# Performance work log

Measured on AMD Instinct MI355X. Metric: run time of the kernel, lower is better.

Reference implementation:

```python
import jax, jax.numpy as jnp
import numpy as np

B, S, D, H = 4, 2048, 768, 12
HD = D // H  # head_dim = 64


def setup_inputs() -> dict:
    key = jax.random.key(0)
    k1, k2, k3, k4, k5 = jax.random.split(key, 5)
    scale = 0.02
    return {
        "x": jax.random.normal(k1, (B, S, D), dtype=jnp.float32),
        "w_qkv": jax.random.normal(k2, (D, 3 * D), dtype=jnp.float32) * scale,
        "b_qkv": jax.random.normal(k3, (3 * D,), dtype=jnp.float32) * scale,
        "w_proj": jax.random.normal(k4, (D, D), dtype=jnp.float32) * scale,
        "b_proj": jax.random.normal(k5, (D,), dtype=jnp.float32) * scale,
    }


def reference(x, w_qkv, b_qkv, w_proj, b_proj):
    b, s, d = x.shape
    # fused qkv projection: (b, s, 3d) -> (3, b, h, s, hd)
    qkv = x @ w_qkv + b_qkv
    qkv = qkv.reshape(b, s, 3, H, HD).transpose(2, 0, 3, 1, 4)
    q, k, v = qkv[0], qkv[1], qkv[2]
    # scaled dot-product attention with explicit (b, h, s, s) scores
    scores = jnp.einsum("bhqd,bhkd->bhqk", q, k) / jnp.sqrt(jnp.float32(HD))
    attn = jax.nn.softmax(scores, axis=-1)
    out = jnp.einsum("bhqk,bhkd->bhqd", attn, v)
    out = out.transpose(0, 2, 1, 3).reshape(b, s, d)  # concat heads
    return out @ w_proj + b_proj
```

## Files before the change

kernel.cpp:

```cpp
#include <hip/hip_runtime.h>
#include <hip/hip_bf16.h>
#include <stdint.h>


typedef __attribute__((ext_vector_type(8))) short bf16x8;
typedef __attribute__((ext_vector_type(4))) float f32x4;
typedef __attribute__((ext_vector_type(4))) unsigned short u16x4;

__device__ __forceinline__ unsigned short f2bf(float x) {
  union { float f; uint32_t u; } v; v.f = x;
  uint32_t r = v.u + 0x7FFF + ((v.u >> 16) & 1);
  return (unsigned short)(r >> 16);
}

__device__ __forceinline__ uint32_t cvtpk_bf16(float lo, float hi) {
  uint32_t r;
  asm("v_cvt_pk_bf16_f32 %0, %1, %2" : "=v"(r) : "v"(lo), "v"(hi));
  return r;
}

__device__ __forceinline__ void gload_lds16(const void* g, void* l) {
  __builtin_amdgcn_global_load_lds(
      (const __attribute__((address_space(1))) void*)g,
      (__attribute__((address_space(3))) void*)l, 16, 0, 0);
}

__global__ void cast_x_kernel(const float* __restrict__ x,
                              unsigned short* __restrict__ xb, int n) {
  int idx = (blockIdx.x * blockDim.x + threadIdx.x) * 4;
  if (idx < n) {
    f32x4 v = *(const f32x4*)(x + idx);
    u16x4 o;
    o[0] = f2bf(v[0]); o[1] = f2bf(v[1]); o[2] = f2bf(v[2]); o[3] = f2bf(v[3]);
    *(u16x4*)(xb + idx) = o;
  }
}

__global__ void transpose_cast_kernel(const float* __restrict__ W,
                                      unsigned short* __restrict__ Wt,
                                      int K, int N) {
  __shared__ float tile[64][65];
  int k0 = blockIdx.y * 64, n0 = blockIdx.x * 64;
  int t = threadIdx.x;
#pragma unroll
  for (int i = 0; i < 16; i++) {
    int idx = i * 256 + t; int r = idx >> 6, c = idx & 63;
    tile[r][c] = W[(size_t)(k0 + r) * N + n0 + c];
  }
  __syncthreads();
#pragma unroll
  for (int i = 0; i < 16; i++) {
    int idx = i * 256 + t; int r = idx >> 6, c = idx & 63;
    Wt[(size_t)(n0 + r) * K + k0 + c] = f2bf(tile[c][r]);
  }
}

template <int EPI>
__global__ __launch_bounds__(256, 2) void gemm_kernel(
    const unsigned short* __restrict__ A,
    const unsigned short* __restrict__ Bt,
    const float* __restrict__ bias,
    void* __restrict__ out0,
    unsigned short* __restrict__ Kb,
    unsigned short* __restrict__ Vt,
    int M, int N, int K) {
  __shared__ unsigned short As[128 * 64];
  __shared__ unsigned short Bs[128 * 64];
  const int tid = threadIdx.x;
  const int wave = tid >> 6, lane = tid & 63;
  const int wm = wave >> 1, wn = wave & 1;
  const int m0 = blockIdx.y * 128, n0 = blockIdx.x * 128;
  const int g = lane >> 4, c16 = lane & 15;
  f32x4 acc[4][4] = {};

  for (int k0 = 0; k0 < K; k0 += 64) {
    int rb = wave * 32;
#pragma unroll
    for (int j = 0; j < 4; j++) {
      int r = rb + j * 8 + (lane >> 3);
      int ca = (lane & 7) ^ (r & 7);
      gload_lds16(A + (size_t)(m0 + r) * K + k0 + ca * 8, As + (rb + j * 8) * 64);
      gload_lds16(Bt + (size_t)(n0 + r) * K + k0 + ca * 8, Bs + (rb + j * 8) * 64);
    }
    __syncthreads();
#pragma unroll
    for (int ks = 0; ks < 2; ks++) {
      bf16x8 af[4], bfr[4];
#pragma unroll
      for (int mi = 0; mi < 4; mi++) {
        int row = wm * 64 + mi * 16 + c16;
        int ch = (ks * 4 + g) ^ (row & 7);
        af[mi] = *(const bf16x8*)(As + row * 64 + ch * 8);
      }
#pragma unroll
      for (int nj = 0; nj < 4; nj++) {
        int row = wn * 64 + nj * 16 + c16;
        int ch = (ks * 4 + g) ^ (row & 7);
        bfr[nj] = *(const bf16x8*)(Bs + row * 64 + ch * 8);
      }
#pragma unroll
      for (int mi = 0; mi < 4; mi++)
#pragma unroll
        for (int nj = 0; nj < 4; nj++)
          acc[mi][nj] = __builtin_amdgcn_mfma_f32_16x16x32_bf16(
              af[mi], bfr[nj], acc[mi][nj], 0, 0, 0);
    }
    __syncthreads();
  }

  if (EPI == 0) {
    const float QSC = 0.125f * 1.44269504088896f;
    unsigned short* Qb = (unsigned short*)out0;
#pragma unroll
    for (int nj = 0; nj < 4; nj++) {
      int n = n0 + wn * 64 + nj * 16 + c16;
      int t = n / 768, rr = n % 768;
      int h = rr >> 6, d = rr & 63;
      float bv = bias[n];
#pragma unroll
      for (int mi = 0; mi < 4; mi++) {
        int mrow = m0 + wm * 64 + mi * 16 + g * 4;
        int b = mrow >> 11, s = mrow & 2047;
        if (t == 0) {
          size_t base = ((size_t)(b * 12 + h) * 2048 + s) * 64 + d;
#pragma unroll
          for (int rg = 0; rg < 4; rg++)
            Qb[base + (size_t)rg * 64] = f2bf((acc[mi][nj][rg] + bv) * QSC);
        } else if (t == 1) {
          size_t base = ((size_t)(b * 12 + h) * 2048 + s) * 64 + d;
#pragma unroll
          for (int rg = 0; rg < 4; rg++)
            Kb[base + (size_t)rg * 64] = f2bf(acc[mi][nj][rg] + bv);
        } else {
          int sp = (s & ~31) + (((s >> 2) & 3) << 3) + (((s >> 4) & 1) << 2);
          u16x4 p;
          p[0] = f2bf(acc[mi][nj][0] + bv);
          p[1] = f2bf(acc[mi][nj][1] + bv);
          p[2] = f2bf(acc[mi][nj][2] + bv);
          p[3] = f2bf(acc[mi][nj][3] + bv);
          *(u16x4*)(Vt + ((size_t)(b * 12 + h) * 64 + d) * 2048 + sp) = p;
        }
      }
    }
  } else {
    float* outp = (float*)out0;
#pragma unroll
    for (int nj = 0; nj < 4; nj++) {
      int n = n0 + wn * 64 + nj * 16 + c16;
      float bv = bias[n];
#pragma unroll
      for (int mi = 0; mi < 4; mi++) {
        int mrow = m0 + wm * 64 + mi * 16 + g * 4;
#pragma unroll
        for (int rg = 0; rg < 4; rg++)
          outp[(size_t)(mrow + rg) * N + n] = acc[mi][nj][rg] + bv;
      }
    }
  }
}

__global__ __launch_bounds__(256, 4) void attn_kernel(
    const unsigned short* __restrict__ Qb,
    const unsigned short* __restrict__ Kb,
    const unsigned short* __restrict__ Vt,
    unsigned short* __restrict__ Ao) {
  __shared__ unsigned short Ks[64 * 64];
  __shared__ unsigned short Vs[64 * 64];
  const int id = blockIdx.x;
  const int xcd = id & 7, slot = id >> 3;
  const int bh = xcd * 6 + (slot % 6);
  const int q0 = (slot / 6) * 128;
  const int tid = threadIdx.x;
  const int wave = tid >> 6, lane = tid & 63;
  const int g = lane >> 4, c16 = lane & 15;
  const int rw = c16 & 7;
  const int rb = wave * 16;

  const int sr = rb + (lane >> 3);
  const int sca = (lane & 7) ^ (sr & 7);
  const unsigned short* kp = Kb + ((size_t)bh * 2048 + sr) * 64 + sca * 8;
  const unsigned short* vp = Vt + ((size_t)bh * 64 + sr) * 2048 + sca * 8;

  bf16x8 qf[2][2];
  {
    const unsigned short* qp =
        Qb + ((size_t)bh * 2048 + q0 + wave * 32 + c16) * 64;
#pragma unroll
    for (int qa = 0; qa < 2; qa++) {
      qf[qa][0] = *(const bf16x8*)(qp + qa * 1024 + g * 8);
      qf[qa][1] = *(const bf16x8*)(qp + qa * 1024 + 32 + g * 8);
    }
  }
  f32x4 acc_o[2][4] = {};
  float l_run[2] = {0.f, 0.f};
  const int alane = (lane & 48) + g * 4;

  for (int kt = 0; kt < 32; kt++) {
    gload_lds16(kp, Ks + rb * 64);
    gload_lds16(kp + 8 * 64, Ks + (rb + 8) * 64);
    gload_lds16(vp, Vs + rb * 64);
    gload_lds16(vp + 8 * 2048, Vs + (rb + 8) * 64);
    kp += 64 * 64;
    vp += 64;
    __syncthreads();

    f32x4 sacc[2][4] = {};
#pragma unroll
    for (int ks = 0; ks < 2; ks++) {
#pragma unroll
      for (int nf = 0; nf < 4; nf++) {
        int row = nf * 16 + c16;
        int ch = (ks * 4 + g) ^ (row & 7);
        bf16x8 kf = *(const bf16x8*)(Ks + row * 64 + ch * 8);
        sacc[0][nf] =
            __builtin_amdgcn_mfma_f32_16x16x32_bf16(kf, qf[0][ks], sacc[0][nf], 0, 0, 0);
        sacc[1][nf] =
            __builtin_amdgcn_mfma_f32_16x16x32_bf16(kf, qf[1][ks], sacc[1][nf], 0, 0, 0);
      }
    }

#pragma unroll
    for (int qa = 0; qa < 2; qa++) {
      float rs = 0.f;
#pragma unroll
      for (int nf = 0; nf < 4; nf++) {
        sacc[qa][nf][0] = __builtin_amdgcn_exp2f(sacc[qa][nf][0]);
        sacc[qa][nf][1] = __builtin_amdgcn_exp2f(sacc[qa][nf][1]);
        sacc[qa][nf][2] = __builtin_amdgcn_exp2f(sacc[qa][nf][2]);
        sacc[qa][nf][3] = __builtin_amdgcn_exp2f(sacc[qa][nf][3]);
        rs += (sacc[qa][nf][0] + sacc[qa][nf][1]) +
              (sacc[qa][nf][2] + sacc[qa][nf][3]);
      }
      l_run[qa] += rs;
    }

#pragma unroll
    for (int ks = 0; ks < 2; ks++) {
      union { uint32_t w[4]; bf16x8 v8; } pa0, pa1;
      pa0.w[0] = cvtpk_bf16(sacc[0][2 * ks][0], sacc[0][2 * ks][1]);
      pa0.w[1] = cvtpk_bf16(sacc[0][2 * ks][2], sacc[0][2 * ks][3]);
      pa0.w[2] = cvtpk_bf16(sacc[0][2 * ks + 1][0], sacc[0][2 * ks + 1][1]);
      pa0.w[3] = cvtpk_bf16(sacc[0][2 * ks + 1][2], sacc[0][2 * ks + 1][3]);
      pa1.w[0] = cvtpk_bf16(sacc[1][2 * ks][0], sacc[1][2 * ks][1]);
      pa1.w[1] = cvtpk_bf16(sacc[1][2 * ks][2], sacc[1][2 * ks][3]);
      pa1.w[2] = cvtpk_bf16(sacc[1][2 * ks + 1][0], sacc[1][2 * ks + 1][1]);
      pa1.w[3] = cvtpk_bf16(sacc[1][2 * ks + 1][2], sacc[1][2 * ks + 1][3]);
#pragma unroll
      for (int nf = 0; nf < 4; nf++) {
        int row = nf * 16 + c16;
        int ch = (ks * 4 + g) ^ rw;
        bf16x8 vf = *(const bf16x8*)(&Vs[row * 64 + ch * 8]);
        acc_o[0][nf] =
            __builtin_amdgcn_mfma_f32_16x16x32_bf16(pa0.v8, vf, acc_o[0][nf], 0, 0, 0);
        acc_o[1][nf] =
            __builtin_amdgcn_mfma_f32_16x16x32_bf16(pa1.v8, vf, acc_o[1][nf], 0, 0, 0);
      }
    }
    __syncthreads();
  }

  const int b = bh / 12, h = bh % 12;
#pragma unroll
  for (int qa = 0; qa < 2; qa++) {
    float t = l_run[qa];
    t += __shfl_xor(t, 16);
    t += __shfl_xor(t, 32);
    float l_q[4];
#pragma unroll
    for (int rg = 0; rg < 4; rg++)
      l_q[rg] = __shfl(t, alane + rg);
#pragma unroll
    for (int nf = 0; nf < 4; nf++) {
#pragma unroll
      for (int rg = 0; rg < 4; rg++) {
        float v = acc_o[qa][nf][rg] / l_q[rg];
        int srow = q0 + wave * 32 + qa * 16 + g * 4 + rg;
        Ao[((size_t)(b * 2048 + srow)) * 768 + h * 64 + nf * 16 + c16] = f2bf(v);
      }
    }
  }
}

extern "C" void kernel_launch(void* const* d_in, const int* in_sizes, int n_in,
                              void* d_out, int out_size, void* d_ws, size_t ws_size,
                              hipStream_t stream) {
  const float* x      = (const float*)d_in[0];
  const float* w_qkv  = (const float*)d_in[1];
  const float* b_qkv  = (const float*)d_in[2];
  const float* w_proj = (const float*)d_in[3];
  const float* b_proj = (const float*)d_in[4];

  unsigned short* xb  = (unsigned short*)d_ws;
  unsigned short* wqt = xb + 6291456;
  unsigned short* wpt = wqt + 1769472;
  unsigned short* Qb  = wpt + 589824;
  unsigned short* Kb  = Qb + 6291456;
  unsigned short* Vt  = Kb + 6291456;
  unsigned short* Ao  = Vt + 6291456;

  cast_x_kernel<<<6144, 256, 0, stream>>>(x, xb, 6291456);
  transpose_cast_kernel<<<dim3(36, 12), 256, 0, stream>>>(w_qkv, wqt, 768, 2304);
  transpose_cast_kernel<<<dim3(12, 12), 256, 0, stream>>>(w_proj, wpt, 768, 768);

  gemm_kernel<0><<<dim3(18, 64), 256, 0, stream>>>(
      xb, wqt, b_qkv, (void*)Qb, Kb, Vt, 8192, 2304, 768);

  attn_kernel<<<768, 256, 0, stream>>>(Qb, Kb, Vt, Ao);

  gemm_kernel<1><<<dim3(6, 64), 256, 0, stream>>>(
      Ao, wpt, b_proj, d_out, nullptr, nullptr, 8192, 768, 768);
}
```

Before: 143.7 us.

## Use two waves per attention block with 64 query rows per wave

The attention kernel drops from four waves to two per 128-query block, and each wave now handles 64 query rows instead of 32. Each K/V fragment read from LDS is reused across four query sub-tiles instead of two, so LDS read traffic per MFMA is halved. Each wave also issues twice as many global-to-LDS loads per tile. The cost is higher register pressure from the larger accumulators, plus fewer waves per block and a launch bound of 2, which may reduce occupancy and latency hiding.

```diff
diff --git a/kernel.cpp b/kernel.cpp
--- a/kernel.cpp
+++ b/kernel.cpp
@@ -159,7 +159,7 @@
   }
 }
 
-__global__ __launch_bounds__(256, 4) void attn_kernel(
+__global__ __launch_bounds__(128, 2) void attn_kernel(
     const unsigned short* __restrict__ Qb,
     const unsigned short* __restrict__ Kb,
     const unsigned short* __restrict__ Vt,
@@ -174,37 +174,40 @@
   const int wave = tid >> 6, lane = tid & 63;
   const int g = lane >> 4, c16 = lane & 15;
   const int rw = c16 & 7;
-  const int rb = wave * 16;
-
-  const int sr = rb + (lane >> 3);
+
+  const int sr = wave * 32 + (lane >> 3);
   const int sca = (lane & 7) ^ (sr & 7);
   const unsigned short* kp = Kb + ((size_t)bh * 2048 + sr) * 64 + sca * 8;
   const unsigned short* vp = Vt + ((size_t)bh * 64 + sr) * 2048 + sca * 8;
 
-  bf16x8 qf[2][2];
+  bf16x8 qf[4][2];
   {
     const unsigned short* qp =
-        Qb + ((size_t)bh * 2048 + q0 + wave * 32 + c16) * 64;
-#pragma unroll
-    for (int qa = 0; qa < 2; qa++) {
+        Qb + ((size_t)bh * 2048 + q0 + wave * 64 + c16) * 64;
+#pragma unroll
+    for (int qa = 0; qa < 4; qa++) {
       qf[qa][0] = *(const bf16x8*)(qp + qa * 1024 + g * 8);
       qf[qa][1] = *(const bf16x8*)(qp + qa * 1024 + 32 + g * 8);
     }
   }
-  f32x4 acc_o[2][4] = {};
-  float l_run[2] = {0.f, 0.f};
+  f32x4 acc_o[4][4] = {};
+  float l_run[4] = {0.f, 0.f, 0.f, 0.f};
   const int alane = (lane & 48) + g * 4;
 
   for (int kt = 0; kt < 32; kt++) {
-    gload_lds16(kp, Ks + rb * 64);
-    gload_lds16(kp + 8 * 64, Ks + (rb + 8) * 64);
-    gload_lds16(vp, Vs + rb * 64);
-    gload_lds16(vp + 8 * 2048, Vs + (rb + 8) * 64);
+    gload_lds16(kp, Ks + (wave * 32) * 64);
+    gload_lds16(kp + 8 * 64, Ks + (wave * 32 + 8) * 64);
+    gload_lds16(kp + 16 * 64, Ks + (wave * 32 + 16) * 64);
+    gload_lds16(kp + 24 * 64, Ks + (wave * 32 + 24) * 64);
+    gload_lds16(vp, Vs + (wave * 32) * 64);
+    gload_lds16(vp + 8 * 2048, Vs + (wave * 32 + 8) * 64);
+    gload_lds16(vp + 16 * 2048, Vs + (wave * 32 + 16) * 64);
+    gload_lds16(vp + 24 * 2048, Vs + (wave * 32 + 24) * 64);
     kp += 64 * 64;
     vp += 64;
     __syncthreads();
 
-    f32x4 sacc[2][4] = {};
+    f32x4 sacc[4][4] = {};
 #pragma unroll
     for (int ks = 0; ks < 2; ks++) {
 #pragma unroll
@@ -212,15 +215,15 @@
         int row = nf * 16 + c16;
         int ch = (ks * 4 + g) ^ (row & 7);
         bf16x8 kf = *(const bf16x8*)(Ks + row * 64 + ch * 8);
-        sacc[0][nf] =
-            __builtin_amdgcn_mfma_f32_16x16x32_bf16(kf, qf[0][ks], sacc[0][nf], 0, 0, 0);
-        sacc[1][nf] =
-            __builtin_amdgcn_mfma_f32_16x16x32_bf16(kf, qf[1][ks], sacc[1][nf], 0, 0, 0);
-      }
-    }
-
-#pragma unroll
-    for (int qa = 0; qa < 2; qa++) {
+#pragma unroll
+        for (int qa = 0; qa < 4; qa++)
+          sacc[qa][nf] = __builtin_amdgcn_mfma_f32_16x16x32_bf16(
+              kf, qf[qa][ks], sacc[qa][nf], 0, 0, 0);
+      }
+    }
+
+#pragma unroll
+    for (int qa = 0; qa < 4; qa++) {
       float rs = 0.f;
 #pragma unroll
       for (int nf = 0; nf < 4; nf++) {
@@ -236,24 +239,23 @@
 
 #pragma unroll
     for (int ks = 0; ks < 2; ks++) {
-      union { uint32_t w[4]; bf16x8 v8; } pa0, pa1;
-      pa0.w[0] = cvtpk_bf16(sacc[0][2 * ks][0], sacc[0][2 * ks][1]);
-      pa0.w[1] = cvtpk_bf16(sacc[0][2 * ks][2], sacc[0][2 * ks][3]);
-      pa0.w[2] = cvtpk_bf16(sacc[0][2 * ks + 1][0], sacc[0][2 * ks + 1][1]);
-      pa0.w[3] = cvtpk_bf16(sacc[0][2 * ks + 1][2], sacc[0][2 * ks + 1][3]);
-      pa1.w[0] = cvtpk_bf16(sacc[1][2 * ks][0], sacc[1][2 * ks][1]);
-      pa1.w[1] = cvtpk_bf16(sacc[1][2 * ks][2], sacc[1][2 * ks][3]);
-      pa1.w[2] = cvtpk_bf16(sacc[1][2 * ks + 1][0], sacc[1][2 * ks + 1][1]);
-      pa1.w[3] = cvtpk_bf16(sacc[1][2 * ks + 1][2], sacc[1][2 * ks + 1][3]);
+      union { uint32_t w[4]; bf16x8 v8; } pa[4];
+#pragma unroll
+      for (int qa = 0; qa < 4; qa++) {
+        pa[qa].w[0] = cvtpk_bf16(sacc[qa][2 * ks][0], sacc[qa][2 * ks][1]);
+        pa[qa].w[1] = cvtpk_bf16(sacc[qa][2 * ks][2], sacc[qa][2 * ks][3]);
+        pa[qa].w[2] = cvtpk_bf16(sacc[qa][2 * ks + 1][0], sacc[qa][2 * ks + 1][1]);
+        pa[qa].w[3] = cvtpk_bf16(sacc[qa][2 * ks + 1][2], sacc[qa][2 * ks + 1][3]);
+      }
 #pragma unroll
       for (int nf = 0; nf < 4; nf++) {
         int row = nf * 16 + c16;
         int ch = (ks * 4 + g) ^ rw;
         bf16x8 vf = *(const bf16x8*)(&Vs[row * 64 + ch * 8]);
-        acc_o[0][nf] =
-            __builtin_amdgcn_mfma_f32_16x16x32_bf16(pa0.v8, vf, acc_o[0][nf], 0, 0, 0);
-        acc_o[1][nf] =
-            __builtin_amdgcn_mfma_f32_16x16x32_bf16(pa1.v8, vf, acc_o[1][nf], 0, 0, 0);
+#pragma unroll
+        for (int qa = 0; qa < 4; qa++)
+          acc_o[qa][nf] = __builtin_amdgcn_mfma_f32_16x16x32_bf16(
+              pa[qa].v8, vf, acc_o[qa][nf], 0, 0, 0);
       }
     }
     __syncthreads();
@@ -261,7 +263,7 @@
 
   const int b = bh / 12, h = bh % 12;
 #pragma unroll
-  for (int qa = 0; qa < 2; qa++) {
+  for (int qa = 0; qa < 4; qa++) {
     float t = l_run[qa];
     t += __shfl_xor(t, 16);
     t += __shfl_xor(t, 32);
@@ -274,7 +276,7 @@
 #pragma unroll
       for (int rg = 0; rg < 4; rg++) {
         float v = acc_o[qa][nf][rg] / l_q[rg];
-        int srow = q0 + wave * 32 + qa * 16 + g * 4 + rg;
+        int srow = q0 + wave * 64 + qa * 16 + g * 4 + rg;
         Ao[((size_t)(b * 2048 + srow)) * 768 + h * 64 + nf * 16 + c16] = f2bf(v);
       }
     }
@@ -305,7 +307,7 @@
   gemm_kernel<0><<<dim3(18, 64), 256, 0, stream>>>(
       xb, wqt, b_qkv, (void*)Qb, Kb, Vt, 8192, 2304, 768);
 
-  attn_kernel<<<768, 256, 0, stream>>>(Qb, Kb, Vt, Ao);
+  attn_kernel<<<768, 128, 0, stream>>>(Qb, Kb, Vt, Ao);
 
   gemm_kernel<1><<<dim3(6, 64), 256, 0, stream>>>(
       Ao, wpt, b_proj, d_out, nullptr, nullptr, 8192, 768, 768);
```

Result: slower. 154.0 us (+7.2%).
